# Optimization experiments

Hardware: AMD Instinct MI355X
Metric: run time of the kernel (lower is better)

Reference implementation:

```python
import jax, jax.numpy as jnp
import numpy as np

B, H, S, D = 2, 16, 2048, 64

def setup_inputs() -> dict:
    key = jax.random.key(0)
    kq, kk, kv = jax.random.split(key, 3)
    q = jax.random.normal(kq, (B, H, S, D), dtype=jnp.float32)
    k = jax.random.normal(kk, (B, H, S, D), dtype=jnp.float32)
    v = jax.random.normal(kv, (B, H, S, D), dtype=jnp.float32)
    # causal mask: True where position j > i (future tokens are masked)
    mask = jnp.triu(jnp.ones((S, S), dtype=bool), k=1)[None, None, :, :]
    return {"q": q, "k": k, "v": v, "mask": mask}

def reference(q, k, v, mask) -> jnp.ndarray:
    # scaled dot-product attention with additive -1e4 mask bias
    scale = 1.0 / jnp.sqrt(jnp.asarray(q.shape[-1], q.dtype))
    scores = jnp.einsum('bhqd,bhkd->bhqk', q, k) * scale  # [B,H,S,S]
    scores = scores + mask.astype(scores.dtype) * jnp.asarray(-10000.0, scores.dtype)
    probs = jax.nn.softmax(scores, axis=-1)
    # dropout is identity in eval mode
    return jnp.einsum('bhqk,bhkd->bhqd', probs, v)
```

## Files before the change

### kernel.cpp

```cpp
#include <hip/hip_runtime.h>

typedef __bf16 bf16_t;
typedef bf16_t bf16x8 __attribute__((ext_vector_type(8)));
typedef bf16_t bf16x4 __attribute__((ext_vector_type(4)));
typedef float  floatx4 __attribute__((ext_vector_type(4)));

constexpr int Sq = 2048, Dq = 64;
constexpr int BQ = 64, BK = 64;
constexpr int NQT = Sq / BQ;
constexpr int STR = 72;
constexpr float SCALE_LOG2E = 0.125f * 1.44269504088896340736f;

__global__ __launch_bounds__(256, 2) void flash_attn_kernel(
    const float* __restrict__ Q, const float* __restrict__ K,
    const float* __restrict__ V, float* __restrict__ O)
{
    __shared__ bf16_t QPs[BQ][STR];
    __shared__ bf16_t Ks[2][BK][STR];
    __shared__ bf16_t VTs[2][Dq][STR];

    const int tid  = threadIdx.x;
    const int wave = tid >> 6;
    const int lane = tid & 63;
    const int quad = lane >> 4;
    const int l16  = lane & 15;

    const int id = blockIdx.x;
    const int bh = (id & 7) + ((id >> 7) << 3);
    const int pr = (id >> 3) & 15;
    const long base = (long)bh * Sq * Dq;

    const int r0 = tid >> 4;
    const int c4 = (tid & 15) * 4;
    const int h  = lane >> 3;
    const int jw = wave * 16;

    for (int half = 0; half < 2; ++half) {
        const int qt = half ? (NQT - 1 - pr) : pr;

        __syncthreads();
        #pragma unroll
        for (int p = 0; p < 4; ++p) {
            const int row = p * 16 + r0;
            const float4 qv = *(const float4*)&Q[base + (long)(qt * BQ + row) * Dq + c4];
            bf16x4 w;
            w[0] = (bf16_t)(qv.x * SCALE_LOG2E); w[1] = (bf16_t)(qv.y * SCALE_LOG2E);
            w[2] = (bf16_t)(qv.z * SCALE_LOG2E); w[3] = (bf16_t)(qv.w * SCALE_LOG2E);
            *(bf16x4*)&QPs[row][c4] = w;
        }
        __syncthreads();

        bf16x8 aq0, aq1;
        {
            const int qrow = wave * 16 + l16;
            aq0 = *(const bf16x8*)&QPs[qrow][quad * 8];
            aq1 = *(const bf16x8*)&QPs[qrow][32 + quad * 8];
        }

        float l_lane = 0.f;
        floatx4 o_acc[4];
        #pragma unroll
        for (int i = 0; i < 4; ++i) o_acc[i] = floatx4{0.f, 0.f, 0.f, 0.f};

        {
            #pragma unroll
            for (int p = 0; p < 4; ++p) {
                const float4 kv = *(const float4*)&K[base + (long)(p * 16 + r0) * Dq + c4];
                bf16x4 w;
                w[0] = (bf16_t)kv.x; w[1] = (bf16_t)kv.y;
                w[2] = (bf16_t)kv.z; w[3] = (bf16_t)kv.w;
                *(bf16x4*)&Ks[0][p * 16 + r0][c4] = w;
                const int j0 = jw + 4 * ((p + h) & 3);
                bf16x4 vw;
                #pragma unroll
                for (int r = 0; r < 4; ++r)
                    vw[r] = (bf16_t)V[base + (long)(j0 + r) * Dq + lane];
                *(bf16x4*)&VTs[0][lane][j0] = vw;
            }
        }
        __syncthreads();

        for (int kt = 0; kt <= qt; ++kt) {
            const int cur  = kt & 1;
            const bool more = (kt < qt);

            float4 kf[4];
            float  vf[4][4];
            if (more) {
                const long kb = base + (long)(kt + 1) * BK * Dq;
                #pragma unroll
                for (int p = 0; p < 4; ++p) {
                    kf[p] = *(const float4*)&K[kb + (long)(p * 16 + r0) * Dq + c4];
                    const int j0 = jw + 4 * ((p + h) & 3);
                    #pragma unroll
                    for (int r = 0; r < 4; ++r)
                        vf[p][r] = V[kb + (long)(j0 + r) * Dq + lane];
                }
            }

            floatx4 acc[4];
            __builtin_amdgcn_s_setprio(1);
            #pragma unroll
            for (int t = 0; t < 4; ++t) {
                acc[t] = floatx4{0.f, 0.f, 0.f, 0.f};
                const int krow = t * 16 + l16;
                bf16x8 ak0 = *(const bf16x8*)&Ks[cur][krow][quad * 8];
                bf16x8 ak1 = *(const bf16x8*)&Ks[cur][krow][32 + quad * 8];
                acc[t] = __builtin_amdgcn_mfma_f32_16x16x32_bf16(ak0, aq0, acc[t], 0, 0, 0);
                acc[t] = __builtin_amdgcn_mfma_f32_16x16x32_bf16(ak1, aq1, acc[t], 0, 0, 0);
            }
            __builtin_amdgcn_s_setprio(0);

            if (kt == qt) {
                const int qr = wave * 16 + l16;
                #pragma unroll
                for (int t = 0; t < 4; ++t) {
                    #pragma unroll
                    for (int i = 0; i < 4; ++i) {
                        if (t * 16 + quad * 4 + i > qr) acc[t][i] = -1e30f;
                    }
                }
            }

            float esum[4];
            #pragma unroll
            for (int t = 0; t < 4; ++t) {
                #pragma unroll
                for (int i = 0; i < 4; ++i)
                    acc[t][i] = __builtin_amdgcn_exp2f(acc[t][i]);
                esum[t] = (acc[t][0] + acc[t][1]) + (acc[t][2] + acc[t][3]);
            }
            l_lane += (esum[0] + esum[1]) + (esum[2] + esum[3]);

            #pragma unroll
            for (int t = 0; t < 4; ++t) {
                bf16x4 pk;
                pk[0] = (bf16_t)acc[t][0]; pk[1] = (bf16_t)acc[t][1];
                pk[2] = (bf16_t)acc[t][2]; pk[3] = (bf16_t)acc[t][3];
                *(bf16x4*)&QPs[wave * 16 + l16][t * 16 + quad * 4] = pk;
            }

            bf16x8 ap0 = *(const bf16x8*)&QPs[wave * 16 + l16][quad * 8];
            bf16x8 ap1 = *(const bf16x8*)&QPs[wave * 16 + l16][32 + quad * 8];
            __builtin_amdgcn_s_setprio(1);
            #pragma unroll
            for (int dt = 0; dt < 4; ++dt) {
                const int dcol = dt * 16 + l16;
                bf16x8 bv0 = *(const bf16x8*)&VTs[cur][dcol][quad * 8];
                bf16x8 bv1 = *(const bf16x8*)&VTs[cur][dcol][32 + quad * 8];
                o_acc[dt] = __builtin_amdgcn_mfma_f32_16x16x32_bf16(ap0, bv0, o_acc[dt], 0, 0, 0);
                o_acc[dt] = __builtin_amdgcn_mfma_f32_16x16x32_bf16(ap1, bv1, o_acc[dt], 0, 0, 0);
            }
            __builtin_amdgcn_s_setprio(0);

            if (more) {
                #pragma unroll
                for (int p = 0; p < 4; ++p) {
                    bf16x4 w;
                    w[0] = (bf16_t)kf[p].x; w[1] = (bf16_t)kf[p].y;
                    w[2] = (bf16_t)kf[p].z; w[3] = (bf16_t)kf[p].w;
                    *(bf16x4*)&Ks[cur ^ 1][p * 16 + r0][c4] = w;
                    bf16x4 vw;
                    vw[0] = (bf16_t)vf[p][0]; vw[1] = (bf16_t)vf[p][1];
                    vw[2] = (bf16_t)vf[p][2]; vw[3] = (bf16_t)vf[p][3];
                    *(bf16x4*)&VTs[cur ^ 1][lane][jw + 4 * ((p + h) & 3)] = vw;
                }
                __syncthreads();
            }
        }

        float lsum = l_lane;
        lsum += __shfl_xor(lsum, 16);
        lsum += __shfl_xor(lsum, 32);
        #pragma unroll
        for (int i = 0; i < 4; ++i) {
            const float inv_l = 1.f / __shfl(lsum, quad * 4 + i, 16);
            const long row = (long)qt * BQ + wave * 16 + quad * 4 + i;
            #pragma unroll
            for (int dt = 0; dt < 4; ++dt) {
                O[base + row * Dq + dt * 16 + l16] = o_acc[dt][i] * inv_l;
            }
        }
    }
}

extern "C" void kernel_launch(void* const* d_in, const int* in_sizes, int n_in,
                              void* d_out, int out_size, void* d_ws, size_t ws_size,
                              hipStream_t stream)
{
    const float* q = (const float*)d_in[0];
    const float* k = (const float*)d_in[1];
    const float* v = (const float*)d_in[2];
    float* out = (float*)d_out;
    flash_attn_kernel<<<dim3(512, 1, 1), dim3(256, 1, 1), 0, stream>>>(q, k, v, out);
}
```

Measured before the change: 131.2 us.

## Widen query tile to 128 rows, one tile per block

Doubles the query tile to 128 rows so each wave owns two 16-row slices that share every K/V tile loaded into shared memory. This halves the K/V global loads and bf16 conversions per query row. It drops the paired light/heavy tile scheme: each block now processes a single causal tile, and ordering alternates across block groups. The cost is more accumulator registers under the same launch bounds and a much less even workload per block, since the longest block now does roughly twice as much matrix work per iteration.

```diff
diff --git a/kernel.cpp b/kernel.cpp
--- a/kernel.cpp
+++ b/kernel.cpp
@@ -6,7 +6,7 @@
 typedef float  floatx4 __attribute__((ext_vector_type(4)));
 
 constexpr int Sq = 2048, Dq = 64;
-constexpr int BQ = 64, BK = 64;
+constexpr int BQ = 128, BK = 64;
 constexpr int NQT = Sq / BQ;
 constexpr int STR = 72;
 constexpr float SCALE_LOG2E = 0.125f * 1.44269504088896340736f;
@@ -25,9 +25,11 @@
     const int quad = lane >> 4;
     const int l16  = lane & 15;
 
-    const int id = blockIdx.x;
-    const int bh = (id & 7) + ((id >> 7) << 3);
-    const int pr = (id >> 3) & 15;
+    const int id   = blockIdx.x;
+    const int g    = id >> 7;
+    const int bh   = (id & 7) + (g << 3);
+    const int slot = (id >> 3) & 15;
+    const int qt   = ((g >> 1) & 1) ? slot : (NQT - 1 - slot);
     const long base = (long)bh * Sq * Dq;
 
     const int r0 = tid >> 4;
@@ -35,150 +37,172 @@
     const int h  = lane >> 3;
     const int jw = wave * 16;
 
-    for (int half = 0; half < 2; ++half) {
-        const int qt = half ? (NQT - 1 - pr) : pr;
-
-        __syncthreads();
+    #pragma unroll
+    for (int p = 0; p < 8; ++p) {
+        const int row = p * 16 + r0;
+        const float4 qv = *(const float4*)&Q[base + (long)(qt * BQ + row) * Dq + c4];
+        bf16x4 w;
+        w[0] = (bf16_t)(qv.x * SCALE_LOG2E); w[1] = (bf16_t)(qv.y * SCALE_LOG2E);
+        w[2] = (bf16_t)(qv.z * SCALE_LOG2E); w[3] = (bf16_t)(qv.w * SCALE_LOG2E);
+        *(bf16x4*)&QPs[row][c4] = w;
+    }
+    __syncthreads();
+
+    bf16x8 aq0[2], aq1[2];
+    #pragma unroll
+    for (int s = 0; s < 2; ++s) {
+        const int qrow = wave * 32 + s * 16 + l16;
+        aq0[s] = *(const bf16x8*)&QPs[qrow][quad * 8];
+        aq1[s] = *(const bf16x8*)&QPs[qrow][32 + quad * 8];
+    }
+
+    float l_lane[2] = {0.f, 0.f};
+    floatx4 o_acc[2][4];
+    #pragma unroll
+    for (int s = 0; s < 2; ++s)
+        #pragma unroll
+        for (int i = 0; i < 4; ++i) o_acc[s][i] = floatx4{0.f, 0.f, 0.f, 0.f};
+
+    {
         #pragma unroll
         for (int p = 0; p < 4; ++p) {
-            const int row = p * 16 + r0;
-            const float4 qv = *(const float4*)&Q[base + (long)(qt * BQ + row) * Dq + c4];
+            const float4 kv = *(const float4*)&K[base + (long)(p * 16 + r0) * Dq + c4];
             bf16x4 w;
-            w[0] = (bf16_t)(qv.x * SCALE_LOG2E); w[1] = (bf16_t)(qv.y * SCALE_LOG2E);
-            w[2] = (bf16_t)(qv.z * SCALE_LOG2E); w[3] = (bf16_t)(qv.w * SCALE_LOG2E);
-            *(bf16x4*)&QPs[row][c4] = w;
-        }
-        __syncthreads();
-
-        bf16x8 aq0, aq1;
-        {
-            const int qrow = wave * 16 + l16;
-            aq0 = *(const bf16x8*)&QPs[qrow][quad * 8];
-            aq1 = *(const bf16x8*)&QPs[qrow][32 + quad * 8];
-        }
-
-        float l_lane = 0.f;
-        floatx4 o_acc[4];
-        #pragma unroll
-        for (int i = 0; i < 4; ++i) o_acc[i] = floatx4{0.f, 0.f, 0.f, 0.f};
-
-        {
+            w[0] = (bf16_t)kv.x; w[1] = (bf16_t)kv.y;
+            w[2] = (bf16_t)kv.z; w[3] = (bf16_t)kv.w;
+            *(bf16x4*)&Ks[0][p * 16 + r0][c4] = w;
+            const int j0 = jw + 4 * ((p + h) & 3);
+            bf16x4 vw;
+            #pragma unroll
+            for (int r = 0; r < 4; ++r)
+                vw[r] = (bf16_t)V[base + (long)(j0 + r) * Dq + lane];
+            *(bf16x4*)&VTs[0][lane][j0] = vw;
+        }
+    }
+    __syncthreads();
+
+    const int kmax = 2 * qt + 1;
+    for (int kt = 0; kt <= kmax; ++kt) {
+        const int cur  = kt & 1;
+        const bool more = (kt < kmax);
+
+        float4 kf[4];
+        float  vf[4][4];
+        if (more) {
+            const long kb = base + (long)(kt + 1) * BK * Dq;
             #pragma unroll
             for (int p = 0; p < 4; ++p) {
-                const float4 kv = *(const float4*)&K[base + (long)(p * 16 + r0) * Dq + c4];
-                bf16x4 w;
-                w[0] = (bf16_t)kv.x; w[1] = (bf16_t)kv.y;
-                w[2] = (bf16_t)kv.z; w[3] = (bf16_t)kv.w;
-                *(bf16x4*)&Ks[0][p * 16 + r0][c4] = w;
+                kf[p] = *(const float4*)&K[kb + (long)(p * 16 + r0) * Dq + c4];
                 const int j0 = jw + 4 * ((p + h) & 3);
-                bf16x4 vw;
                 #pragma unroll
                 for (int r = 0; r < 4; ++r)
-                    vw[r] = (bf16_t)V[base + (long)(j0 + r) * Dq + lane];
-                *(bf16x4*)&VTs[0][lane][j0] = vw;
-            }
-        }
-        __syncthreads();
-
-        for (int kt = 0; kt <= qt; ++kt) {
-            const int cur  = kt & 1;
-            const bool more = (kt < qt);
-
-            float4 kf[4];
-            float  vf[4][4];
-            if (more) {
-                const long kb = base + (long)(kt + 1) * BK * Dq;
-                #pragma unroll
-                for (int p = 0; p < 4; ++p) {
-                    kf[p] = *(const float4*)&K[kb + (long)(p * 16 + r0) * Dq + c4];
-                    const int j0 = jw + 4 * ((p + h) & 3);
-                    #pragma unroll
-                    for (int r = 0; r < 4; ++r)
-                        vf[p][r] = V[kb + (long)(j0 + r) * Dq + lane];
-                }
-            }
-
-            floatx4 acc[4];
-            __builtin_amdgcn_s_setprio(1);
-            #pragma unroll
-            for (int t = 0; t < 4; ++t) {
-                acc[t] = floatx4{0.f, 0.f, 0.f, 0.f};
-                const int krow = t * 16 + l16;
-                bf16x8 ak0 = *(const bf16x8*)&Ks[cur][krow][quad * 8];
-                bf16x8 ak1 = *(const bf16x8*)&Ks[cur][krow][32 + quad * 8];
-                acc[t] = __builtin_amdgcn_mfma_f32_16x16x32_bf16(ak0, aq0, acc[t], 0, 0, 0);
-                acc[t] = __builtin_amdgcn_mfma_f32_16x16x32_bf16(ak1, aq1, acc[t], 0, 0, 0);
-            }
-            __builtin_amdgcn_s_setprio(0);
-
-            if (kt == qt) {
-                const int qr = wave * 16 + l16;
+                    vf[p][r] = V[kb + (long)(j0 + r) * Dq + lane];
+            }
+        }
+
+        floatx4 acc[2][4];
+        __builtin_amdgcn_s_setprio(1);
+        #pragma unroll
+        for (int t = 0; t < 4; ++t) {
+            const int krow = t * 16 + l16;
+            bf16x8 ak0 = *(const bf16x8*)&Ks[cur][krow][quad * 8];
+            bf16x8 ak1 = *(const bf16x8*)&Ks[cur][krow][32 + quad * 8];
+            #pragma unroll
+            for (int s = 0; s < 2; ++s) {
+                acc[s][t] = floatx4{0.f, 0.f, 0.f, 0.f};
+                acc[s][t] = __builtin_amdgcn_mfma_f32_16x16x32_bf16(ak0, aq0[s], acc[s][t], 0, 0, 0);
+                acc[s][t] = __builtin_amdgcn_mfma_f32_16x16x32_bf16(ak1, aq1[s], acc[s][t], 0, 0, 0);
+            }
+        }
+        __builtin_amdgcn_s_setprio(0);
+
+        if (kt >= 2 * qt) {
+            const int kbase = (kt - 2 * qt) * 64;
+            #pragma unroll
+            for (int s = 0; s < 2; ++s) {
+                const int qls = wave * 32 + s * 16 + l16;
                 #pragma unroll
                 for (int t = 0; t < 4; ++t) {
                     #pragma unroll
                     for (int i = 0; i < 4; ++i) {
-                        if (t * 16 + quad * 4 + i > qr) acc[t][i] = -1e30f;
+                        if (kbase + t * 16 + quad * 4 + i > qls) acc[s][t][i] = -1e30f;
                     }
                 }
             }
-
+        }
+
+        #pragma unroll
+        for (int s = 0; s < 2; ++s) {
             float esum[4];
             #pragma unroll
             for (int t = 0; t < 4; ++t) {
                 #pragma unroll
                 for (int i = 0; i < 4; ++i)
-                    acc[t][i] = __builtin_amdgcn_exp2f(acc[t][i]);
-                esum[t] = (acc[t][0] + acc[t][1]) + (acc[t][2] + acc[t][3]);
-            }
-            l_lane += (esum[0] + esum[1]) + (esum[2] + esum[3]);
-
+                    acc[s][t][i] = __builtin_amdgcn_exp2f(acc[s][t][i]);
+                esum[t] = (acc[s][t][0] + acc[s][t][1]) + (acc[s][t][2] + acc[s][t][3]);
+            }
+            l_lane[s] += (esum[0] + esum[1]) + (esum[2] + esum[3]);
+        }
+
+        #pragma unroll
+        for (int s = 0; s < 2; ++s) {
             #pragma unroll
             for (int t = 0; t < 4; ++t) {
                 bf16x4 pk;
-                pk[0] = (bf16_t)acc[t][0]; pk[1] = (bf16_t)acc[t][1];
-                pk[2] = (bf16_t)acc[t][2]; pk[3] = (bf16_t)acc[t][3];
-                *(bf16x4*)&QPs[wave * 16 + l16][t * 16 + quad * 4] = pk;
-            }
-
-            bf16x8 ap0 = *(const bf16x8*)&QPs[wave * 16 + l16][quad * 8];
-            bf16x8 ap1 = *(const bf16x8*)&QPs[wave * 16 + l16][32 + quad * 8];
-            __builtin_amdgcn_s_setprio(1);
-            #pragma unroll
-            for (int dt = 0; dt < 4; ++dt) {
-                const int dcol = dt * 16 + l16;
-                bf16x8 bv0 = *(const bf16x8*)&VTs[cur][dcol][quad * 8];
-                bf16x8 bv1 = *(const bf16x8*)&VTs[cur][dcol][32 + quad * 8];
-                o_acc[dt] = __builtin_amdgcn_mfma_f32_16x16x32_bf16(ap0, bv0, o_acc[dt], 0, 0, 0);
-                o_acc[dt] = __builtin_amdgcn_mfma_f32_16x16x32_bf16(ap1, bv1, o_acc[dt], 0, 0, 0);
-            }
-            __builtin_amdgcn_s_setprio(0);
-
-            if (more) {
-                #pragma unroll
-                for (int p = 0; p < 4; ++p) {
-                    bf16x4 w;
-                    w[0] = (bf16_t)kf[p].x; w[1] = (bf16_t)kf[p].y;
-                    w[2] = (bf16_t)kf[p].z; w[3] = (bf16_t)kf[p].w;
-                    *(bf16x4*)&Ks[cur ^ 1][p * 16 + r0][c4] = w;
-                    bf16x4 vw;
-                    vw[0] = (bf16_t)vf[p][0]; vw[1] = (bf16_t)vf[p][1];
-                    vw[2] = (bf16_t)vf[p][2]; vw[3] = (bf16_t)vf[p][3];
-                    *(bf16x4*)&VTs[cur ^ 1][lane][jw + 4 * ((p + h) & 3)] = vw;
-                }
-                __syncthreads();
-            }
-        }
-
-        float lsum = l_lane;
+                pk[0] = (bf16_t)acc[s][t][0]; pk[1] = (bf16_t)acc[s][t][1];
+                pk[2] = (bf16_t)acc[s][t][2]; pk[3] = (bf16_t)acc[s][t][3];
+                *(bf16x4*)&QPs[wave * 32 + s * 16 + l16][t * 16 + quad * 4] = pk;
+            }
+        }
+
+        bf16x8 ap0[2], ap1[2];
+        #pragma unroll
+        for (int s = 0; s < 2; ++s) {
+            ap0[s] = *(const bf16x8*)&QPs[wave * 32 + s * 16 + l16][quad * 8];
+            ap1[s] = *(const bf16x8*)&QPs[wave * 32 + s * 16 + l16][32 + quad * 8];
+        }
+        __builtin_amdgcn_s_setprio(1);
+        #pragma unroll
+        for (int dt = 0; dt < 4; ++dt) {
+            const int dcol = dt * 16 + l16;
+            bf16x8 bv0 = *(const bf16x8*)&VTs[cur][dcol][quad * 8];
+            bf16x8 bv1 = *(const bf16x8*)&VTs[cur][dcol][32 + quad * 8];
+            #pragma unroll
+            for (int s = 0; s < 2; ++s) {
+                o_acc[s][dt] = __builtin_amdgcn_mfma_f32_16x16x32_bf16(ap0[s], bv0, o_acc[s][dt], 0, 0, 0);
+                o_acc[s][dt] = __builtin_amdgcn_mfma_f32_16x16x32_bf16(ap1[s], bv1, o_acc[s][dt], 0, 0, 0);
+            }
+        }
+        __builtin_amdgcn_s_setprio(0);
+
+        if (more) {
+            #pragma unroll
+            for (int p = 0; p < 4; ++p) {
+                bf16x4 w;
+                w[0] = (bf16_t)kf[p].x; w[1] = (bf16_t)kf[p].y;
+                w[2] = (bf16_t)kf[p].z; w[3] = (bf16_t)kf[p].w;
+                *(bf16x4*)&Ks[cur ^ 1][p * 16 + r0][c4] = w;
+                bf16x4 vw;
+                vw[0] = (bf16_t)vf[p][0]; vw[1] = (bf16_t)vf[p][1];
+                vw[2] = (bf16_t)vf[p][2]; vw[3] = (bf16_t)vf[p][3];
+                *(bf16x4*)&VTs[cur ^ 1][lane][jw + 4 * ((p + h) & 3)] = vw;
+            }
+            __syncthreads();
+        }
+    }
+
+    #pragma unroll
+    for (int s = 0; s < 2; ++s) {
+        float lsum = l_lane[s];
         lsum += __shfl_xor(lsum, 16);
         lsum += __shfl_xor(lsum, 32);
         #pragma unroll
         for (int i = 0; i < 4; ++i) {
             const float inv_l = 1.f / __shfl(lsum, quad * 4 + i, 16);
-            const long row = (long)qt * BQ + wave * 16 + quad * 4 + i;
+            const long row = (long)qt * BQ + wave * 32 + s * 16 + quad * 4 + i;
             #pragma unroll
             for (int dt = 0; dt < 4; ++dt) {
-                O[base + row * Dq + dt * 16 + l16] = o_acc[dt][i] * inv_l;
+                O[base + row * Dq + dt * 16 + l16] = o_acc[s][dt][i] * inv_l;
             }
         }
     }
```

Result: slower. 135.9 us (+3.5%).

## Split attention by key slices per wave with register-resident Q and K operands

Applied to the files above, without the earlier changes.

Each wave now owns a 16-key slice of the tile and computes scores for all 64 queries, with Q and K held in registers. This removes the shared-memory staging of Q, K and the P round-trip; probabilities feed a 16x16x16 MFMA directly as the B operand. Partial outputs and row sums from the four waves are reduced through shared memory in the epilogue, which adds extra syncs, LDS traffic, and a 16-tile accumulator per lane (register pressure). The union lets the epilogue buffer reuse the V tile storage.

```diff
diff --git a/kernel.cpp b/kernel.cpp
--- a/kernel.cpp
+++ b/kernel.cpp
@@ -4,6 +4,7 @@
 typedef bf16_t bf16x8 __attribute__((ext_vector_type(8)));
 typedef bf16_t bf16x4 __attribute__((ext_vector_type(4)));
 typedef float  floatx4 __attribute__((ext_vector_type(4)));
+typedef short  shortx4 __attribute__((ext_vector_type(4)));
 
 constexpr int Sq = 2048, Dq = 64;
 constexpr int BQ = 64, BK = 64;
@@ -11,13 +12,30 @@
 constexpr int STR = 72;
 constexpr float SCALE_LOG2E = 0.125f * 1.44269504088896340736f;
 
+struct SmemLoop { bf16_t VTs[2][Dq][STR]; };
+struct SmemEpi  { float Op[4][Dq][17]; float lw[4][16]; };
+union  SmemU    { SmemLoop l; SmemEpi e; };
+
+static __device__ __forceinline__ bf16x8 cvt8(const float4& a, const float4& b) {
+    bf16x8 w;
+    w[0] = (bf16_t)a.x; w[1] = (bf16_t)a.y; w[2] = (bf16_t)a.z; w[3] = (bf16_t)a.w;
+    w[4] = (bf16_t)b.x; w[5] = (bf16_t)b.y; w[6] = (bf16_t)b.z; w[7] = (bf16_t)b.w;
+    return w;
+}
+static __device__ __forceinline__ bf16x8 cvt8s(const float4& a, const float4& b) {
+    bf16x8 w;
+    w[0] = (bf16_t)(a.x * SCALE_LOG2E); w[1] = (bf16_t)(a.y * SCALE_LOG2E);
+    w[2] = (bf16_t)(a.z * SCALE_LOG2E); w[3] = (bf16_t)(a.w * SCALE_LOG2E);
+    w[4] = (bf16_t)(b.x * SCALE_LOG2E); w[5] = (bf16_t)(b.y * SCALE_LOG2E);
+    w[6] = (bf16_t)(b.z * SCALE_LOG2E); w[7] = (bf16_t)(b.w * SCALE_LOG2E);
+    return w;
+}
+
 __global__ __launch_bounds__(256, 2) void flash_attn_kernel(
     const float* __restrict__ Q, const float* __restrict__ K,
     const float* __restrict__ V, float* __restrict__ O)
 {
-    __shared__ bf16_t QPs[BQ][STR];
-    __shared__ bf16_t Ks[2][BK][STR];
-    __shared__ bf16_t VTs[2][Dq][STR];
+    __shared__ SmemU sm;
 
     const int tid  = threadIdx.x;
     const int wave = tid >> 6;
@@ -30,67 +48,79 @@
     const int pr = (id >> 3) & 15;
     const long base = (long)bh * Sq * Dq;
 
-    const int r0 = tid >> 4;
-    const int c4 = (tid & 15) * 4;
-    const int h  = lane >> 3;
-    const int jw = wave * 16;
+    const int h    = lane >> 3;
+    const int jw   = wave * 16;
+    const int c8   = quad * 8;
+    const int krow = 16 * wave + l16;
 
     for (int half = 0; half < 2; ++half) {
         const int qt = half ? (NQT - 1 - pr) : pr;
+        const long qb = base + (long)qt * BQ * Dq;
 
         __syncthreads();
+
+        bf16x8 aq0[4], aq1[4];
+        #pragma unroll
+        for (int u = 0; u < 4; ++u) {
+            const float* qr = &Q[qb + (long)(u * 16 + l16) * Dq];
+            float4 a = *(const float4*)&qr[c8];
+            float4 b = *(const float4*)&qr[c8 + 4];
+            float4 c = *(const float4*)&qr[32 + c8];
+            float4 d = *(const float4*)&qr[32 + c8 + 4];
+            aq0[u] = cvt8s(a, b);
+            aq1[u] = cvt8s(c, d);
+        }
+
+        float4 kraw[4];
+        {
+            const float* kr = &K[base + (long)krow * Dq];
+            kraw[0] = *(const float4*)&kr[c8];
+            kraw[1] = *(const float4*)&kr[c8 + 4];
+            kraw[2] = *(const float4*)&kr[32 + c8];
+            kraw[3] = *(const float4*)&kr[32 + c8 + 4];
+        }
+        float vf[4][4];
         #pragma unroll
         for (int p = 0; p < 4; ++p) {
-            const int row = p * 16 + r0;
-            const float4 qv = *(const float4*)&Q[base + (long)(qt * BQ + row) * Dq + c4];
-            bf16x4 w;
-            w[0] = (bf16_t)(qv.x * SCALE_LOG2E); w[1] = (bf16_t)(qv.y * SCALE_LOG2E);
-            w[2] = (bf16_t)(qv.z * SCALE_LOG2E); w[3] = (bf16_t)(qv.w * SCALE_LOG2E);
-            *(bf16x4*)&QPs[row][c4] = w;
-        }
+            const int j0 = jw + 4 * ((p + h) & 3);
+            #pragma unroll
+            for (int r = 0; r < 4; ++r)
+                vf[p][r] = V[base + (long)(j0 + r) * Dq + lane];
+        }
+        #pragma unroll
+        for (int p = 0; p < 4; ++p) {
+            const int j0 = jw + 4 * ((p + h) & 3);
+            bf16x4 vw;
+            vw[0] = (bf16_t)vf[p][0]; vw[1] = (bf16_t)vf[p][1];
+            vw[2] = (bf16_t)vf[p][2]; vw[3] = (bf16_t)vf[p][3];
+            *(bf16x4*)&sm.l.VTs[0][lane][j0] = vw;
+        }
+        bf16x8 kA0 = cvt8(kraw[0], kraw[1]);
+        bf16x8 kA1 = cvt8(kraw[2], kraw[3]);
+
+        float l_lane[4] = {0.f, 0.f, 0.f, 0.f};
+        floatx4 o_acc[4][4];
+        #pragma unroll
+        for (int dt = 0; dt < 4; ++dt)
+            #pragma unroll
+            for (int u = 0; u < 4; ++u)
+                o_acc[dt][u] = floatx4{0.f, 0.f, 0.f, 0.f};
+
         __syncthreads();
 
-        bf16x8 aq0, aq1;
-        {
-            const int qrow = wave * 16 + l16;
-            aq0 = *(const bf16x8*)&QPs[qrow][quad * 8];
-            aq1 = *(const bf16x8*)&QPs[qrow][32 + quad * 8];
-        }
-
-        float l_lane = 0.f;
-        floatx4 o_acc[4];
-        #pragma unroll
-        for (int i = 0; i < 4; ++i) o_acc[i] = floatx4{0.f, 0.f, 0.f, 0.f};
-
-        {
-            #pragma unroll
-            for (int p = 0; p < 4; ++p) {
-                const float4 kv = *(const float4*)&K[base + (long)(p * 16 + r0) * Dq + c4];
-                bf16x4 w;
-                w[0] = (bf16_t)kv.x; w[1] = (bf16_t)kv.y;
-                w[2] = (bf16_t)kv.z; w[3] = (bf16_t)kv.w;
-                *(bf16x4*)&Ks[0][p * 16 + r0][c4] = w;
-                const int j0 = jw + 4 * ((p + h) & 3);
-                bf16x4 vw;
-                #pragma unroll
-                for (int r = 0; r < 4; ++r)
-                    vw[r] = (bf16_t)V[base + (long)(j0 + r) * Dq + lane];
-                *(bf16x4*)&VTs[0][lane][j0] = vw;
-            }
-        }
-        __syncthreads();
-
         for (int kt = 0; kt <= qt; ++kt) {
-            const int cur  = kt & 1;
+            const int cur   = kt & 1;
             const bool more = (kt < qt);
 
-            float4 kf[4];
-            float  vf[4][4];
             if (more) {
                 const long kb = base + (long)(kt + 1) * BK * Dq;
+                const float* kr = &K[kb + (long)krow * Dq];
+                kraw[0] = *(const float4*)&kr[c8];
+                kraw[1] = *(const float4*)&kr[c8 + 4];
+                kraw[2] = *(const float4*)&kr[32 + c8];
+                kraw[3] = *(const float4*)&kr[32 + c8 + 4];
                 #pragma unroll
                 for (int p = 0; p < 4; ++p) {
-                    kf[p] = *(const float4*)&K[kb + (long)(p * 16 + r0) * Dq + c4];
                     const int j0 = jw + 4 * ((p + h) & 3);
                     #pragma unroll
                     for (int r = 0; r < 4; ++r)
@@ -98,88 +128,101 @@
                 }
             }
 
+            bf16x4 va[4];
+            #pragma unroll
+            for (int dt = 0; dt < 4; ++dt)
+                va[dt] = *(const bf16x4*)&sm.l.VTs[cur][dt * 16 + l16][16 * wave + quad * 4];
+
             floatx4 acc[4];
             __builtin_amdgcn_s_setprio(1);
             #pragma unroll
-            for (int t = 0; t < 4; ++t) {
-                acc[t] = floatx4{0.f, 0.f, 0.f, 0.f};
-                const int krow = t * 16 + l16;
-                bf16x8 ak0 = *(const bf16x8*)&Ks[cur][krow][quad * 8];
-                bf16x8 ak1 = *(const bf16x8*)&Ks[cur][krow][32 + quad * 8];
-                acc[t] = __builtin_amdgcn_mfma_f32_16x16x32_bf16(ak0, aq0, acc[t], 0, 0, 0);
-                acc[t] = __builtin_amdgcn_mfma_f32_16x16x32_bf16(ak1, aq1, acc[t], 0, 0, 0);
+            for (int u = 0; u < 4; ++u) {
+                acc[u] = floatx4{0.f, 0.f, 0.f, 0.f};
+                acc[u] = __builtin_amdgcn_mfma_f32_16x16x32_bf16(kA0, aq0[u], acc[u], 0, 0, 0);
+                acc[u] = __builtin_amdgcn_mfma_f32_16x16x32_bf16(kA1, aq1[u], acc[u], 0, 0, 0);
             }
             __builtin_amdgcn_s_setprio(0);
 
             if (kt == qt) {
-                const int qr = wave * 16 + l16;
-                #pragma unroll
-                for (int t = 0; t < 4; ++t) {
+                const int kl = 16 * wave + quad * 4;
+                #pragma unroll
+                for (int u = 0; u < 4; ++u) {
+                    const int ql = u * 16 + l16;
                     #pragma unroll
-                    for (int i = 0; i < 4; ++i) {
-                        if (t * 16 + quad * 4 + i > qr) acc[t][i] = -1e30f;
-                    }
+                    for (int i = 0; i < 4; ++i)
+                        if (kl + i > ql) acc[u][i] = -1e30f;
                 }
             }
 
-            float esum[4];
-            #pragma unroll
-            for (int t = 0; t < 4; ++t) {
+            shortx4 pb[4];
+            #pragma unroll
+            for (int u = 0; u < 4; ++u) {
                 #pragma unroll
                 for (int i = 0; i < 4; ++i)
-                    acc[t][i] = __builtin_amdgcn_exp2f(acc[t][i]);
-                esum[t] = (acc[t][0] + acc[t][1]) + (acc[t][2] + acc[t][3]);
-            }
-            l_lane += (esum[0] + esum[1]) + (esum[2] + esum[3]);
-
-            #pragma unroll
-            for (int t = 0; t < 4; ++t) {
+                    acc[u][i] = __builtin_amdgcn_exp2f(acc[u][i]);
+                l_lane[u] += (acc[u][0] + acc[u][1]) + (acc[u][2] + acc[u][3]);
                 bf16x4 pk;
-                pk[0] = (bf16_t)acc[t][0]; pk[1] = (bf16_t)acc[t][1];
-                pk[2] = (bf16_t)acc[t][2]; pk[3] = (bf16_t)acc[t][3];
-                *(bf16x4*)&QPs[wave * 16 + l16][t * 16 + quad * 4] = pk;
-            }
-
-            bf16x8 ap0 = *(const bf16x8*)&QPs[wave * 16 + l16][quad * 8];
-            bf16x8 ap1 = *(const bf16x8*)&QPs[wave * 16 + l16][32 + quad * 8];
+                pk[0] = (bf16_t)acc[u][0]; pk[1] = (bf16_t)acc[u][1];
+                pk[2] = (bf16_t)acc[u][2]; pk[3] = (bf16_t)acc[u][3];
+                pb[u] = __builtin_bit_cast(shortx4, pk);
+            }
+
             __builtin_amdgcn_s_setprio(1);
             #pragma unroll
             for (int dt = 0; dt < 4; ++dt) {
-                const int dcol = dt * 16 + l16;
-                bf16x8 bv0 = *(const bf16x8*)&VTs[cur][dcol][quad * 8];
-                bf16x8 bv1 = *(const bf16x8*)&VTs[cur][dcol][32 + quad * 8];
-                o_acc[dt] = __builtin_amdgcn_mfma_f32_16x16x32_bf16(ap0, bv0, o_acc[dt], 0, 0, 0);
-                o_acc[dt] = __builtin_amdgcn_mfma_f32_16x16x32_bf16(ap1, bv1, o_acc[dt], 0, 0, 0);
+                const shortx4 vs = __builtin_bit_cast(shortx4, va[dt]);
+                #pragma unroll
+                for (int u = 0; u < 4; ++u)
+                    o_acc[dt][u] = __builtin_amdgcn_mfma_f32_16x16x16bf16_1k(vs, pb[u], o_acc[dt][u], 0, 0, 0);
             }
             __builtin_amdgcn_s_setprio(0);
 
             if (more) {
+                kA0 = cvt8(kraw[0], kraw[1]);
+                kA1 = cvt8(kraw[2], kraw[3]);
                 #pragma unroll
                 for (int p = 0; p < 4; ++p) {
-                    bf16x4 w;
-                    w[0] = (bf16_t)kf[p].x; w[1] = (bf16_t)kf[p].y;
-                    w[2] = (bf16_t)kf[p].z; w[3] = (bf16_t)kf[p].w;
-                    *(bf16x4*)&Ks[cur ^ 1][p * 16 + r0][c4] = w;
+                    const int j0 = jw + 4 * ((p + h) & 3);
                     bf16x4 vw;
                     vw[0] = (bf16_t)vf[p][0]; vw[1] = (bf16_t)vf[p][1];
                     vw[2] = (bf16_t)vf[p][2]; vw[3] = (bf16_t)vf[p][3];
-                    *(bf16x4*)&VTs[cur ^ 1][lane][jw + 4 * ((p + h) & 3)] = vw;
+                    *(bf16x4*)&sm.l.VTs[cur ^ 1][lane][j0] = vw;
                 }
                 __syncthreads();
             }
         }
 
-        float lsum = l_lane;
-        lsum += __shfl_xor(lsum, 16);
-        lsum += __shfl_xor(lsum, 32);
-        #pragma unroll
-        for (int i = 0; i < 4; ++i) {
-            const float inv_l = 1.f / __shfl(lsum, quad * 4 + i, 16);
-            const long row = (long)qt * BQ + wave * 16 + quad * 4 + i;
-            #pragma unroll
-            for (int dt = 0; dt < 4; ++dt) {
-                O[base + row * Dq + dt * 16 + l16] = o_acc[dt][i] * inv_l;
-            }
+        float lw[4];
+        #pragma unroll
+        for (int u = 0; u < 4; ++u) {
+            float t = l_lane[u];
+            t += __shfl_xor(t, 16);
+            t += __shfl_xor(t, 32);
+            lw[u] = t;
+        }
+        __syncthreads();
+
+        const int d_ep = tid & 63;
+        const int q0   = tid >> 6;
+        #pragma unroll
+        for (int u = 0; u < 4; ++u) {
+            #pragma unroll
+            for (int dt = 0; dt < 4; ++dt)
+                #pragma unroll
+                for (int i = 0; i < 4; ++i)
+                    sm.e.Op[wave][dt * 16 + quad * 4 + i][l16] = o_acc[dt][u][i];
+            if (quad == 0) sm.e.lw[wave][l16] = lw[u];
+            __syncthreads();
+            #pragma unroll
+            for (int qq = 0; qq < 4; ++qq) {
+                const int q = q0 + 4 * qq;
+                const float v = sm.e.Op[0][d_ep][q] + sm.e.Op[1][d_ep][q]
+                              + sm.e.Op[2][d_ep][q] + sm.e.Op[3][d_ep][q];
+                const float l = sm.e.lw[0][q] + sm.e.lw[1][q]
+                              + sm.e.lw[2][q] + sm.e.lw[3][q];
+                O[qb + (long)(u * 16 + q) * Dq + d_ep] = v / l;
+            }
+            __syncthreads();
         }
     }
 }
```

Result: slower. 139.8 us (+6.5%).
